# Kernel tuning notes

Measured on AMD Instinct MI355X. Metric: run time of the kernel, lower is better.

## Reference

```python
import jax, jax.numpy as jnp
import numpy as np
import math

B, S, HID = 2, 2048, 1024
NH = 16
HD = HID // NH  # 64
CHUNK = 128  # min(128, S) from the module


def setup_inputs() -> dict:
    key = jax.random.key(0)
    ks = jax.random.split(key, 8)
    scale = 1.0 / math.sqrt(HID)
    return {
        "hidden_states": jax.random.normal(ks[0], (B, S, HID), jnp.float32),
        "attention_mask": jnp.zeros((B, S, S), jnp.float32),
        "Wq": jax.random.normal(ks[1], (HID, HID), jnp.float32) * scale,
        "bq": jnp.zeros((HID,), jnp.float32),
        "Wk": jax.random.normal(ks[2], (HID, HID), jnp.float32) * scale,
        "bk": jnp.zeros((HID,), jnp.float32),
        "Wv": jax.random.normal(ks[3], (HID, HID), jnp.float32) * scale,
        "bv": jnp.zeros((HID,), jnp.float32),
        "head_weights": jnp.ones((NH,), jnp.float32),
    }


def _split_heads(x):
    # [B,S,HID] -> [B,NH,S,HD]
    b, s, _ = x.shape
    return x.reshape(b, s, NH, HD).transpose(0, 2, 1, 3)


def reference(hidden_states, attention_mask, Wq, bq, Wk, bk, Wv, bv, head_weights):
    # nn.Linear: y = x @ W.T + b
    q = _split_heads(hidden_states @ Wq.T + bq)  # [B,NH,S,HD]
    k = _split_heads(hidden_states @ Wk.T + bk)
    v = _split_heads(hidden_states @ Wv.T + bv)

    scores = jnp.einsum("bhqd,bhkd->bhqk", q, k) / math.sqrt(HD)
    scores = scores + attention_mask[:, None, :, :]  # additive mask broadcast over heads
    probs = jax.nn.softmax(scores, axis=-1)
    # dropout p=0.0 -> identity; post-softmax head-weight scaling (head_pruning)
    probs = probs * head_weights[None, :, None, None]
    ctx = jnp.einsum("bhqk,bhkd->bhqd", probs, v)  # [B,NH,S,HD]
    context_layer = ctx.transpose(0, 2, 1, 3).reshape(B, S, HID)

    # module returns the probs of the LAST query chunk of the python loop
    last_start = ((S + CHUNK - 1) // CHUNK - 1) * CHUNK
    output_attention_probs = probs[:, :, last_start:S, :]  # [B,NH,128,S]
    return context_layer, output_attention_probs
```

## Files before the change

kernel.cpp:

```cpp
#include <hip/hip_runtime.h>

typedef unsigned short u16;
typedef __attribute__((ext_vector_type(8))) short bf16x8;
typedef __attribute__((ext_vector_type(4))) float f32x4;

#define B_   2
#define S_   2048
#define HID_ 1024
#define NH_  16
#define HD_  64
#define SCALE_ 0.125f
#define C2_   0.18033688011112f
#define CLAMP2_ 115.4156035f
#define LOG2E_ 1.4426950408890f

__device__ __forceinline__ u16 f2bf(float f) {
    union { float f; unsigned int i; } v; v.f = f;
    unsigned int r = v.i + 0x7fffu + ((v.i >> 16) & 1u);
    return (u16)(r >> 16);
}
__device__ __forceinline__ bf16x8 ld8(const u16* p) {
    return *reinterpret_cast<const bf16x8*>(p);
}
__device__ __forceinline__ unsigned cvtpk(float lo, float hi) {
    unsigned r;
    asm("v_cvt_pk_bf16_f32 %0, %1, %2" : "=v"(r) : "v"(lo), "v"(hi));
    return r;
}
__device__ __forceinline__ float ex2(float x) {
    float r;
    asm("v_exp_f32 %0, %1" : "=v"(r) : "v"(x));
    return r;
}
__device__ __forceinline__ void gll16(const u16* g, const u16* l) {
    __builtin_amdgcn_global_load_lds(
        (const __attribute__((address_space(1))) unsigned int*)g,
        (__attribute__((address_space(3))) unsigned int*)l, 16, 0, 0);
}

__global__ __launch_bounds__(256) void conv_scan(
    const float* __restrict__ X, const float* __restrict__ W0,
    const float* __restrict__ W1, const float* __restrict__ W2,
    const unsigned* __restrict__ m,
    u16* __restrict__ Xb, u16* __restrict__ Wb, unsigned* __restrict__ flag)
{
    const int bx = blockIdx.x;
    if (bx < 3584) {
        const size_t s = (size_t)bx * 256 + threadIdx.x;
        const float* src; u16* dst; size_t off;
        if (s < 524288) { src = X; dst = Xb; off = s * 8; }
        else {
            const size_t t = s - 524288;
            const int w = (int)(t >> 17);
            off = (t & 131071) * 8;
            src = w == 0 ? W0 : w == 1 ? W1 : W2;
            dst = Wb + (size_t)w * 1048576;
        }
        f32x4 a = *(const f32x4*)(src + off);
        f32x4 b = *(const f32x4*)(src + off + 4);
        bf16x8 r;
        #pragma unroll
        for (int e = 0; e < 4; e++) { r[e] = (short)f2bf(a[e]); r[4 + e] = (short)f2bf(b[e]); }
        *(bf16x8*)(dst + off) = r;
    } else {
        const size_t i = ((size_t)(bx - 3584) * 256 + threadIdx.x) * 8;
        const uint4* p = (const uint4*)(m + i);
        uint4 a = p[0], b = p[1];
        const unsigned M = 0x7fffffffu;
        unsigned v = (a.x & M) | (a.y & M) | (a.z & M) | (a.w & M)
                   | (b.x & M) | (b.y & M) | (b.z & M) | (b.w & M);
        if (v) atomicOr(flag, 1u);
    }
}

#define BK_ 32

__global__ __launch_bounds__(256) void qkv_mfma(
    const u16* __restrict__ Xb, const u16* __restrict__ Wb,
    const float* __restrict__ bq, const float* __restrict__ bk,
    const float* __restrict__ bv,
    u16* __restrict__ Q, u16* __restrict__ K, u16* __restrict__ V)
{
    __shared__ __align__(16) u16 As[128 * BK_];
    __shared__ __align__(16) u16 Bs[128 * BK_];

    const int tid  = threadIdx.x;
    const int wave = tid >> 6;
    const int lane = tid & 63;
    const int l16  = lane & 15;
    const int quad = lane >> 4;
    const int wr   = wave >> 1, wc = wave & 1;

    const int i0 = blockIdx.x * 128;
    const int j0 = blockIdx.y * 128;

    const int grow = (wave * 64 + lane) >> 2;
    const int gcol = (lane & 3) * 8;
    const u16* ldsA0 = As + wave * 512;
    const u16* ldsA1 = As + 2048 + wave * 512;
    const u16* ldsB0 = Bs + wave * 512;
    const u16* ldsB1 = Bs + 2048 + wave * 512;

    f32x4 acc[4][4] = {};

    for (int k0 = 0; k0 < HID_; k0 += BK_) {
        __syncthreads();
        gll16(Xb + (size_t)(i0 + grow) * HID_ + k0 + gcol, ldsA0);
        gll16(Xb + (size_t)(i0 + 64 + grow) * HID_ + k0 + gcol, ldsA1);
        gll16(Wb + (size_t)(j0 + grow) * HID_ + k0 + gcol, ldsB0);
        gll16(Wb + (size_t)(j0 + 64 + grow) * HID_ + k0 + gcol, ldsB1);
        __syncthreads();

        bf16x8 af[4], bfr[4];
        #pragma unroll
        for (int mt = 0; mt < 4; mt++)
            af[mt] = ld8(&As[(wr * 64 + mt * 16 + l16) * BK_ + quad * 8]);
        #pragma unroll
        for (int nt = 0; nt < 4; nt++)
            bfr[nt] = ld8(&Bs[(wc * 64 + nt * 16 + l16) * BK_ + quad * 8]);
        #pragma unroll
        for (int mt = 0; mt < 4; mt++)
            #pragma unroll
            for (int nt = 0; nt < 4; nt++)
                acc[mt][nt] = __builtin_amdgcn_mfma_f32_16x16x32_bf16(af[mt], bfr[nt], acc[mt][nt], 0, 0, 0);
    }

    const int which = j0 >> 10;
    const float* bias = which == 0 ? bq : which == 1 ? bk : bv;
    u16* Y            = which == 0 ? Q  : which == 1 ? K  : V;
    const float scl   = which == 0 ? C2_ : 1.0f;

    u16* bb = (wave < 2) ? (As + wave * 2048) : (Bs + (wave - 2) * 2048);

    #pragma unroll
    for (int p = 0; p < 2; p++) {
        __syncthreads();
        #pragma unroll
        for (int t2 = 0; t2 < 2; t2++) {
            const int nt = 2 * p + t2;
            const int j  = j0 + wc * 64 + nt * 16 + l16;
            const int jj = j & 1023;
            const float bv_ = bias[jj];
            #pragma unroll
            for (int mt = 0; mt < 4; mt++)
                #pragma unroll
                for (int r = 0; r < 4; r++) {
                    const int row = mt * 16 + quad * 4 + r;
                    const int col = t2 * 16 + l16;
                    const u16 val = f2bf((acc[mt][nt][r] + bv_) * scl);
                    if (which == 2)
                        bb[col * 64 + (row ^ ((col & 7) << 3))] = val;
                    else
                        bb[row * 32 + (col ^ ((row & 0xC) << 1))] = val;
                }
        }
        __syncthreads();
        #pragma unroll
        for (int k = 0; k < 4; k++) {
            const int c = lane + 64 * k;
            if (which == 2) {
                const int col  = c >> 3;
                const int row0 = (c & 7) * 8;
                bf16x8 v = ld8(&bb[col * 64 + (row0 ^ ((col & 7) << 3))]);
                const int j  = j0 + wc * 64 + p * 32 + col;
                const int jj = j & 1023;
                const int h = jj >> 6, d = jj & 63;
                const int i = i0 + wr * 64 + row0;
                const int b = i >> 11, s = i & (S_ - 1);
                *(bf16x8*)&Y[((size_t)(b * NH_ + h) * HD_ + d) * S_ + s] = v;
            } else {
                const int row  = c >> 2;
                const int col0 = (c & 3) * 8;
                bf16x8 v = ld8(&bb[row * 32 + (col0 ^ ((row & 0xC) << 1))]);
                const int j  = j0 + wc * 64 + p * 32 + col0;
                const int jj = j & 1023;
                const int h = jj >> 6, d = jj & 63;
                const int i = i0 + wr * 64 + row;
                const int b = i >> 11, s = i & (S_ - 1);
                *(bf16x8*)&Y[(((size_t)(b * NH_ + h) * S_ + s) * HD_) + d] = v;
            }
        }
    }
}

__global__ __launch_bounds__(256) void attn(
    const u16* __restrict__ Q, const u16* __restrict__ K, const u16* __restrict__ Vt,
    const float* __restrict__ mask, const float* __restrict__ hw,
    const unsigned* __restrict__ mflag,
    float* __restrict__ ctx, float* __restrict__ ml)
{
    __shared__ __align__(16) u16 Ks[2][64 * 64];
    __shared__ __align__(16) u16 Vs[2][64 * 64];
    __shared__ __align__(16) u16 Pl[4][16 * 64];

    const int usemask = (mflag[0] != 0);

    const int tid  = threadIdx.x;
    const int wave = tid >> 6;
    const int lane = tid & 63;
    const int l16  = lane & 15;
    const int quad = lane >> 4;
    const int x7   = l16 & 7;

    const int lin = blockIdx.x + 32 * (blockIdx.y + 16 * blockIdx.z);
    const int xcd = lin & 7, jj = lin >> 3;
    const int qb  = jj & 31;
    const int hb  = xcd * 4 + (jj >> 5);
    const int h   = hb & 15, b = hb >> 4;
    const int bh  = b * NH_ + h;

    const u16* Qh  = Q  + (size_t)bh * S_ * HD_;
    const u16* Kh  = K  + (size_t)bh * S_ * HD_;
    const u16* Vth = Vt + (size_t)bh * HD_ * S_;
    const float* Mb = mask + (size_t)b * S_ * S_;

    const int q0 = qb * 64 + wave * 16;

    bf16x8 qf0 = ld8(Qh + (size_t)(q0 + l16) * HD_ + quad * 8);
    bf16x8 qf1 = ld8(Qh + (size_t)(q0 + l16) * HD_ + 32 + quad * 8);

    bf16x8 ones;
    #pragma unroll
    for (int e = 0; e < 8; e++) ones[e] = (short)0x3F80;

    f32x4 oacc[4] = {};
    f32x4 lacc = {};

    const int srow = tid >> 3;
    const int sch  = tid & 7;
    const int ssw  = (sch ^ (srow & 7)) * 8;
    const int sL   = srow * 64 + ssw;

    {
        bf16x8 k0 = ld8(Kh + (size_t)srow * HD_ + sch * 8);
        bf16x8 k1 = ld8(Kh + (size_t)(srow + 32) * HD_ + sch * 8);
        bf16x8 v0 = ld8(Vth + (size_t)srow * S_ + sch * 8);
        bf16x8 v1 = ld8(Vth + (size_t)(srow + 32) * S_ + sch * 8);
        *(bf16x8*)&Ks[0][sL] = k0; *(bf16x8*)&Ks[0][sL + 2048] = k1;
        *(bf16x8*)&Vs[0][sL] = v0; *(bf16x8*)&Vs[0][sL + 2048] = v1;
    }
    __syncthreads();

    for (int t = 0; t < 32; ++t) {
        const int cur = t & 1;
        const int kt  = t * 64;
        const u16* Kb = Ks[cur];
        const u16* Vb = Vs[cur];

        bf16x8 kr0, kr1, vr0, vr1;
        if (t < 31) {
            const u16* Kg = Kh + (size_t)(kt + 64) * HD_;
            kr0 = ld8(Kg + (size_t)srow * HD_ + sch * 8);
            kr1 = ld8(Kg + (size_t)(srow + 32) * HD_ + sch * 8);
            vr0 = ld8(Vth + (size_t)srow * S_ + kt + 64 + sch * 8);
            vr1 = ld8(Vth + (size_t)(srow + 32) * S_ + kt + 64 + sch * 8);
        }

        f32x4 sacc[4] = {};
        __builtin_amdgcn_s_setprio(1);
        #pragma unroll
        for (int nb = 0; nb < 4; nb++) {
            const int base = (nb * 16 + l16) * 64;
            bf16x8 k0 = ld8(&Kb[base + ((quad ^ x7) * 8)]);
            bf16x8 k1 = ld8(&Kb[base + (((quad + 4) ^ x7) * 8)]);
            sacc[nb] = __builtin_amdgcn_mfma_f32_16x16x32_bf16(k0, qf0, sacc[nb], 0, 0, 0);
            sacc[nb] = __builtin_amdgcn_mfma_f32_16x16x32_bf16(k1, qf1, sacc[nb], 0, 0, 0);
        }
        __builtin_amdgcn_s_setprio(0);

        float p[4][4];
        if (usemask) {
            const float* Mrow = Mb + (size_t)(q0 + l16) * S_ + kt;
            #pragma unroll
            for (int nb = 0; nb < 4; nb++) {
                const float4 mv = *(const float4*)(Mrow + nb * 16 + quad * 4);
                p[nb][0] = ex2(fminf(fmaf(mv.x, LOG2E_, sacc[nb][0]), CLAMP2_));
                p[nb][1] = ex2(fminf(fmaf(mv.y, LOG2E_, sacc[nb][1]), CLAMP2_));
                p[nb][2] = ex2(fminf(fmaf(mv.z, LOG2E_, sacc[nb][2]), CLAMP2_));
                p[nb][3] = ex2(fminf(fmaf(mv.w, LOG2E_, sacc[nb][3]), CLAMP2_));
            }
        } else {
            #pragma unroll
            for (int nb = 0; nb < 4; nb++)
                #pragma unroll
                for (int r = 0; r < 4; r++)
                    p[nb][r] = ex2(fminf(sacc[nb][r], CLAMP2_));
        }

        {
            u16* prow = &Pl[wave][l16 * 64];
            #pragma unroll
            for (int nb = 0; nb < 4; nb++) {
                uint2 w;
                w.x = cvtpk(p[nb][0], p[nb][1]);
                w.y = cvtpk(p[nb][2], p[nb][3]);
                const int ch  = 2 * nb + (quad >> 1);
                const int off = ((ch ^ x7) << 3) + ((quad & 1) << 2);
                *(uint2*)&prow[off] = w;
            }
        }

        __builtin_amdgcn_s_setprio(1);
        #pragma unroll
        for (int kb = 0; kb < 2; kb++) {
            const int c = kb * 4 + quad;
            bf16x8 pf = ld8(&Pl[wave][l16 * 64 + ((c ^ x7) * 8)]);
            lacc = __builtin_amdgcn_mfma_f32_16x16x32_bf16(pf, ones, lacc, 0, 0, 0);
            #pragma unroll
            for (int db = 0; db < 4; db++) {
                bf16x8 vf = ld8(&Vb[(db * 16 + l16) * 64 + ((c ^ x7) * 8)]);
                oacc[db] = __builtin_amdgcn_mfma_f32_16x16x32_bf16(pf, vf, oacc[db], 0, 0, 0);
            }
        }
        __builtin_amdgcn_s_setprio(0);

        if (t < 31) {
            u16* Kd = Ks[cur ^ 1]; u16* Vd = Vs[cur ^ 1];
            *(bf16x8*)&Kd[sL] = kr0; *(bf16x8*)&Kd[sL + 2048] = kr1;
            *(bf16x8*)&Vd[sL] = vr0; *(bf16x8*)&Vd[sL + 2048] = vr1;
        }
        __syncthreads();
    }

    const float hwf = hw[h];
    float invl[4];
    #pragma unroll
    for (int r = 0; r < 4; r++) invl[r] = hwf / lacc[r];

    #pragma unroll
    for (int db = 0; db < 4; db++)
        #pragma unroll
        for (int r = 0; r < 4; r++) {
            const int qrow = q0 + quad * 4 + r;
            ctx[((size_t)(b * S_ + qrow)) * HID_ + h * HD_ + db * 16 + l16] =
                oacc[db][r] * invl[r];
        }

    if (qb >= 30 && l16 == 0) {
        #pragma unroll
        for (int r = 0; r < 4; r++)
            ml[bh * 128 + (q0 - 1920) + quad * 4 + r] = lacc[r];
    }
}

__global__ __launch_bounds__(256) void probs_qk(
    const u16* __restrict__ Q, const u16* __restrict__ K,
    const float* __restrict__ mask, const float* __restrict__ hw,
    const unsigned* __restrict__ mflag, const float* __restrict__ ml,
    float* __restrict__ probs_out)
{
    const int usemask = (mflag[0] != 0);

    const int tid  = threadIdx.x;
    const int wave = tid >> 6;
    const int lane = tid & 63;
    const int l16  = lane & 15;
    const int quad = lane >> 4;

    const int rt = blockIdx.x & 1;
    const int ks = blockIdx.x >> 1;
    const int h  = blockIdx.y;
    const int b  = blockIdx.z;
    const int bh = b * NH_ + h;

    const u16* Qh = Q + (size_t)bh * S_ * HD_;
    const u16* Kh = K + (size_t)bh * S_ * HD_;
    const float* Mb = mask + (size_t)b * S_ * S_;

    const int q0   = 1920 + rt * 64 + wave * 16;
    const int qrow = q0 + l16;

    bf16x8 qf0 = ld8(Qh + (size_t)qrow * HD_ + quad * 8);
    bf16x8 qf1 = ld8(Qh + (size_t)qrow * HD_ + 32 + quad * 8);

    const float invl = hw[h] / ml[bh * 128 + (qrow - 1920)];
    float* Prow = probs_out + ((size_t)bh * 128 + (qrow - 1920)) * S_;
    const float* Mrow = Mb + (size_t)qrow * S_;

    for (int kt = ks * 256; kt < ks * 256 + 256; kt += 64) {
        f32x4 sacc[4] = {};
        #pragma unroll
        for (int nb = 0; nb < 4; nb++) {
            const u16* krow = Kh + (size_t)(kt + nb * 16 + l16) * HD_ + quad * 8;
            bf16x8 kA0 = ld8(krow);
            bf16x8 kA1 = ld8(krow + 32);
            sacc[nb] = __builtin_amdgcn_mfma_f32_16x16x32_bf16(kA0, qf0, sacc[nb], 0, 0, 0);
            sacc[nb] = __builtin_amdgcn_mfma_f32_16x16x32_bf16(kA1, qf1, sacc[nb], 0, 0, 0);
        }
        #pragma unroll
        for (int nb = 0; nb < 4; nb++) {
            const int kb0 = kt + nb * 16 + quad * 4;
            float4 v;
            if (usemask) {
                const float4 mv = *(const float4*)&Mrow[kb0];
                v.x = ex2(fminf(fmaf(mv.x, LOG2E_, sacc[nb][0]), CLAMP2_)) * invl;
                v.y = ex2(fminf(fmaf(mv.y, LOG2E_, sacc[nb][1]), CLAMP2_)) * invl;
                v.z = ex2(fminf(fmaf(mv.z, LOG2E_, sacc[nb][2]), CLAMP2_)) * invl;
                v.w = ex2(fminf(fmaf(mv.w, LOG2E_, sacc[nb][3]), CLAMP2_)) * invl;
            } else {
                v.x = ex2(fminf(sacc[nb][0], CLAMP2_)) * invl;
                v.y = ex2(fminf(sacc[nb][1], CLAMP2_)) * invl;
                v.z = ex2(fminf(sacc[nb][2], CLAMP2_)) * invl;
                v.w = ex2(fminf(sacc[nb][3], CLAMP2_)) * invl;
            }
            *(float4*)&Prow[kb0] = v;
        }
    }
}

extern "C" void kernel_launch(void* const* d_in, const int* in_sizes, int n_in,
                              void* d_out, int out_size, void* d_ws, size_t ws_size,
                              hipStream_t stream)
{
    const void* X = 0; const void* mask = 0; const void* hw = 0;
    const void* Wm[3] = {0, 0, 0}; const void* bm[3] = {0, 0, 0};
    int wi = 0, bi = 0;
    for (int i = 0; i < n_in; i++) {
        switch (in_sizes[i]) {
            case 4194304: X = d_in[i]; break;
            case 8388608: mask = d_in[i]; break;
            case 1048576: if (wi < 3) Wm[wi++] = d_in[i]; break;
            case 1024:    if (bi < 3) bm[bi++] = d_in[i]; break;
            case 16:      hw = d_in[i]; break;
            default: break;
        }
    }
    if (!X || !mask || wi != 3 || bi != 3 || !hw) {
        X = d_in[0]; mask = d_in[1];
        Wm[0] = d_in[2]; bm[0] = d_in[3];
        Wm[1] = d_in[4]; bm[1] = d_in[5];
        Wm[2] = d_in[6]; bm[2] = d_in[7];
        hw = d_in[8];
    }

    u16* Q  = (u16*)d_ws;
    u16* Kw = Q + 4194304ull;
    u16* Vw = Kw + 4194304ull;
    u16* Xb = Vw + 4194304ull;
    u16* Wb = Xb + 4194304ull;
    unsigned* flag = (unsigned*)(Wb + 3145728ull);
    float* ml = (float*)(flag + 64);

    float* ctx   = (float*)d_out;
    float* probs = ctx + (size_t)B_ * S_ * HID_;

    hipMemsetAsync(flag, 0, 4, stream);
    conv_scan<<<7680, 256, 0, stream>>>(
        (const float*)X, (const float*)Wm[0], (const float*)Wm[1], (const float*)Wm[2],
        (const unsigned*)mask, Xb, Wb, flag);

    qkv_mfma<<<dim3(32, 24), dim3(256), 0, stream>>>(
        Xb, Wb, (const float*)bm[0], (const float*)bm[1], (const float*)bm[2],
        Q, Kw, Vw);

    attn<<<dim3(32, 16, 2), dim3(256), 0, stream>>>(
        Q, Kw, Vw, (const float*)mask, (const float*)hw, flag, ctx, ml);

    probs_qk<<<dim3(16, 16, 2), dim3(256), 0, stream>>>(
        Q, Kw, (const float*)mask, (const float*)hw, flag, ml, probs);
}
```

Measured before the change: 232.8 us.

## Load K/V tiles with direct global-to-LDS loads and pack bf16 conversions

The attention kernel's K/V tile prefetch moves from register staging plus explicit LDS stores to direct global-to-LDS loads (gll16). Each wave fills its own 16-row slice with a pre-swizzled chunk index, which frees the registers held across the compute phase and drops the trailing LDS stores. The cast kernel and the QKV epilogue also switch from scalar f2bf rounding to the packed cvtpk converter. The direct-LDS path relies on the async load finishing before the barrier. gll16 and cvtpk are defined outside the shown diff.

```diff
diff --git a/kernel.cpp b/kernel.cpp
--- a/kernel.cpp
+++ b/kernel.cpp
@@ -58,10 +58,12 @@
         }
         f32x4 a = *(const f32x4*)(src + off);
         f32x4 b = *(const f32x4*)(src + off + 4);
-        bf16x8 r;
-        #pragma unroll
-        for (int e = 0; e < 4; e++) { r[e] = (short)f2bf(a[e]); r[4 + e] = (short)f2bf(b[e]); }
-        *(bf16x8*)(dst + off) = r;
+        uint4 r;
+        r.x = cvtpk(a[0], a[1]);
+        r.y = cvtpk(a[2], a[3]);
+        r.z = cvtpk(b[0], b[1]);
+        r.w = cvtpk(b[2], b[3]);
+        *(uint4*)(dst + off) = r;
     } else {
         const size_t i = ((size_t)(bx - 3584) * 256 + threadIdx.x) * 8;
         const uint4* p = (const uint4*)(m + i);
@@ -141,17 +143,22 @@
             const int j  = j0 + wc * 64 + nt * 16 + l16;
             const int jj = j & 1023;
             const float bv_ = bias[jj];
+            const int col = t2 * 16 + l16;
             #pragma unroll
             for (int mt = 0; mt < 4; mt++)
                 #pragma unroll
-                for (int r = 0; r < 4; r++) {
-                    const int row = mt * 16 + quad * 4 + r;
-                    const int col = t2 * 16 + l16;
-                    const u16 val = f2bf((acc[mt][nt][r] + bv_) * scl);
-                    if (which == 2)
-                        bb[col * 64 + (row ^ ((col & 7) << 3))] = val;
-                    else
-                        bb[row * 32 + (col ^ ((row & 0xC) << 1))] = val;
+                for (int rp = 0; rp < 2; rp++) {
+                    const int row0 = mt * 16 + quad * 4 + 2 * rp;
+                    const unsigned w = cvtpk((acc[mt][nt][2 * rp]     + bv_) * scl,
+                                             (acc[mt][nt][2 * rp + 1] + bv_) * scl);
+                    if (which == 2) {
+                        bb[col * 64 + ( row0      ^ ((col & 7) << 3))] = (u16)w;
+                        bb[col * 64 + ((row0 + 1) ^ ((col & 7) << 3))] = (u16)(w >> 16);
+                    } else {
+                        const int cs = col ^ ((row0 & 0xC) << 1);
+                        bb[ row0      * 32 + cs] = (u16)w;
+                        bb[(row0 + 1) * 32 + cs] = (u16)(w >> 16);
+                    }
                 }
         }
         __syncthreads();
@@ -226,18 +233,15 @@
     f32x4 oacc[4] = {};
     f32x4 lacc = {};
 
-    const int srow = tid >> 3;
-    const int sch  = tid & 7;
-    const int ssw  = (sch ^ (srow & 7)) * 8;
-    const int sL   = srow * 64 + ssw;
+    const int lrow = lane >> 3;
+    const int lchk = ((lane & 7) ^ lrow) * 8;
+    const int u0   = wave * 2;
 
     {
-        bf16x8 k0 = ld8(Kh + (size_t)srow * HD_ + sch * 8);
-        bf16x8 k1 = ld8(Kh + (size_t)(srow + 32) * HD_ + sch * 8);
-        bf16x8 v0 = ld8(Vth + (size_t)srow * S_ + sch * 8);
-        bf16x8 v1 = ld8(Vth + (size_t)(srow + 32) * S_ + sch * 8);
-        *(bf16x8*)&Ks[0][sL] = k0; *(bf16x8*)&Ks[0][sL + 2048] = k1;
-        *(bf16x8*)&Vs[0][sL] = v0; *(bf16x8*)&Vs[0][sL + 2048] = v1;
+        gll16(Kh  + (size_t)(u0 * 8 +     lrow) * HD_ + lchk, &Ks[0][u0 * 512]);
+        gll16(Kh  + (size_t)(u0 * 8 + 8 + lrow) * HD_ + lchk, &Ks[0][u0 * 512 + 512]);
+        gll16(Vth + (size_t)(u0 * 8 +     lrow) * S_  + lchk, &Vs[0][u0 * 512]);
+        gll16(Vth + (size_t)(u0 * 8 + 8 + lrow) * S_  + lchk, &Vs[0][u0 * 512 + 512]);
     }
     __syncthreads();
 
@@ -247,13 +251,12 @@
         const u16* Kb = Ks[cur];
         const u16* Vb = Vs[cur];
 
-        bf16x8 kr0, kr1, vr0, vr1;
         if (t < 31) {
             const u16* Kg = Kh + (size_t)(kt + 64) * HD_;
-            kr0 = ld8(Kg + (size_t)srow * HD_ + sch * 8);
-            kr1 = ld8(Kg + (size_t)(srow + 32) * HD_ + sch * 8);
-            vr0 = ld8(Vth + (size_t)srow * S_ + kt + 64 + sch * 8);
-            vr1 = ld8(Vth + (size_t)(srow + 32) * S_ + kt + 64 + sch * 8);
+            gll16(Kg  + (size_t)(u0 * 8 +     lrow) * HD_ + lchk, &Ks[cur ^ 1][u0 * 512]);
+            gll16(Kg  + (size_t)(u0 * 8 + 8 + lrow) * HD_ + lchk, &Ks[cur ^ 1][u0 * 512 + 512]);
+            gll16(Vth + (size_t)(u0 * 8 +     lrow) * S_ + kt + 64 + lchk, &Vs[cur ^ 1][u0 * 512]);
+            gll16(Vth + (size_t)(u0 * 8 + 8 + lrow) * S_ + kt + 64 + lchk, &Vs[cur ^ 1][u0 * 512 + 512]);
         }
 
         f32x4 sacc[4] = {};
@@ -314,11 +317,6 @@
         }
         __builtin_amdgcn_s_setprio(0);
 
-        if (t < 31) {
-            u16* Kd = Ks[cur ^ 1]; u16* Vd = Vs[cur ^ 1];
-            *(bf16x8*)&Kd[sL] = kr0; *(bf16x8*)&Kd[sL + 2048] = kr1;
-            *(bf16x8*)&Vd[sL] = vr0; *(bf16x8*)&Vd[sL + 2048] = vr1;
-        }
         __syncthreads();
     }
 
```

Measured after the change: 224.3 us. 3.7% less time.
